# Performance work log

Hardware: AMD Instinct MI355X
Metric: run time of the kernel (lower is better)

Reference implementation:

```python
import jax, jax.numpy as jnp
import numpy as np

N_NODES = 50000
N_EDGES = 500000
D_MODEL = 128
EDGE_DIM = 16
LN_EPS = 1e-5


def setup_inputs() -> dict:
    key = jax.random.key(0)
    ks = jax.random.split(key, 12)
    s = 0.05
    return {
        "x_src": jax.random.normal(ks[0], (N_NODES, D_MODEL), jnp.float32),
        "x_dst": jax.random.normal(ks[1], (N_NODES, D_MODEL), jnp.float32),
        "edge_src": jax.random.randint(ks[2], (N_EDGES,), 0, N_NODES, jnp.int32),
        "edge_dst": jax.random.randint(ks[3], (N_EDGES,), 0, N_NODES, jnp.int32),
        "edge_attr": jax.random.normal(ks[4], (N_EDGES, EDGE_DIM), jnp.float32),
        "W_src": jax.random.normal(ks[5], (D_MODEL, D_MODEL), jnp.float32) * s,
        "W_dst": jax.random.normal(ks[6], (D_MODEL, D_MODEL), jnp.float32) * s,
        "b_dst": jnp.zeros((D_MODEL,), jnp.float32),
        "gate_w1": jax.random.normal(ks[7], (D_MODEL, EDGE_DIM), jnp.float32) * s,
        "gate_b1": jnp.zeros((D_MODEL,), jnp.float32),
        "gate_w2": jax.random.normal(ks[8], (1, D_MODEL), jnp.float32) * s,
        "gate_b2": jnp.zeros((1,), jnp.float32),
        "ln_gamma": jnp.ones((D_MODEL,), jnp.float32),
        "ln_beta": jnp.zeros((D_MODEL,), jnp.float32),
    }


def _layernorm(x, gamma, beta):
    mu = jnp.mean(x, axis=-1, keepdims=True)
    var = jnp.mean(jnp.square(x - mu), axis=-1, keepdims=True)
    return (x - mu) * jax.lax.rsqrt(var + LN_EPS) * gamma + beta


def reference(x_src, x_dst, edge_src, edge_dst, edge_attr,
              W_src, W_dst, b_dst, gate_w1, gate_b1, gate_w2, gate_b2,
              ln_gamma, ln_beta):
    n_dst = x_dst.shape[0]
    # gather + linear message: [E, d]
    msg = jnp.einsum('ed,fd->ef', x_src[edge_src], W_src)
    # edge-gate MLP (norm=False, eval mode -> no dropout): Linear -> gelu -> Linear -> sigmoid
    g = jax.nn.gelu(edge_attr @ gate_w1.T + gate_b1, approximate=False)
    gate = jax.nn.sigmoid(g @ gate_w2.T + gate_b2)  # [E, 1]
    msg = msg * gate
    # scatter-add aggregation and degree normalization
    agg = jax.ops.segment_sum(msg, edge_dst, num_segments=n_dst)
    deg = jax.ops.segment_sum(jnp.ones((edge_dst.shape[0],), msg.dtype), edge_dst,
                              num_segments=n_dst)
    agg = agg / jnp.maximum(deg, 1.0)[:, None]
    out = _layernorm(agg + x_dst @ W_dst.T + b_dst, ln_gamma, ln_beta)
    return jax.nn.gelu(out, approximate=False)
```

## Files before the change

### kernel.cpp

```cpp
#include <hip/hip_runtime.h>

#define D_MODEL 128
#define EDGE_DIM 16

typedef __attribute__((ext_vector_type(8))) short bf16x8;
typedef __attribute__((ext_vector_type(4))) float f32x4;

__device__ __forceinline__ float sigmoid_fast(float a) {
    return 1.0f / (1.0f + __expf(-a));
}
__device__ __forceinline__ float gelu_tanh(float x) {
    float x2  = x * x;
    float arg = x * fmaf(0.07135481627f, x2, 1.59576912161f);
    return x * sigmoid_fast(arg);
}

__device__ __forceinline__ float gelu_poly(float x) {
    float s = fminf(x * x, 2.89f);
    float r = fmaf(-9.4447e-6f, s, 1.154347e-4f);
    r = fmaf(r, s, -1.1873282e-3f);
    r = fmaf(r, s, 9.9735570e-3f);
    r = fmaf(r, s, -6.64903801e-2f);
    r = fmaf(r, s, 3.989422804e-1f);
    return fmaf(s, r, 0.5f * x);
}

__device__ __forceinline__ unsigned short f2bf(float x) {
    unsigned u = __float_as_uint(x);
    u += 0x7FFFu + ((u >> 16) & 1u);
    return (unsigned short)(u >> 16);
}

__global__ __launch_bounds__(256) void wt_kernel(
    const float* __restrict__ Wsrc, const float* __restrict__ Wdst,
    unsigned short* __restrict__ wTfrag)
{
    int i = blockIdx.x * 256 + threadIdx.x;
    if (i >= 8 * 8 * 64) return;
    int kc = i >> 9;
    int ft = (i >> 6) & 7;
    int l  = i & 63;
    int f  = ft * 16 + (l & 15);
    int d0 = kc * 32 + (l >> 4) * 8;
    const float* src = (d0 < D_MODEL) ? (Wsrc + (size_t)f * D_MODEL + d0)
                                      : (Wdst + (size_t)f * D_MODEL + (d0 - D_MODEL));
    unsigned short* dst = wTfrag + (size_t)i * 8;
#pragma unroll
    for (int v = 0; v < 8; v++) dst[v] = f2bf(src[v]);
}

__global__ __launch_bounds__(256) void hist_kernel(
    const int* __restrict__ edst, int* __restrict__ degi, int E)
{
    int e = blockIdx.x * 256 + threadIdx.x;
    if (e < E) atomicAdd(&degi[edst[e]], 1);
}

__global__ __launch_bounds__(256) void scan1_kernel(
    const int* __restrict__ degi, int* __restrict__ starts,
    int* __restrict__ partials, int N)
{
    __shared__ int sm[256];
    int t = threadIdx.x;
    int idx = blockIdx.x * 256 + t;
    int val = (idx < N) ? degi[idx] : 0;
    sm[t] = val;
    __syncthreads();
#pragma unroll
    for (int off = 1; off < 256; off <<= 1) {
        int x = (t >= off) ? sm[t - off] : 0;
        __syncthreads();
        sm[t] += x;
        __syncthreads();
    }
    if (idx < N) starts[idx] = sm[t] - val;
    if (t == 255) partials[blockIdx.x] = sm[255];
}

__global__ __launch_bounds__(256) void scan2_kernel(
    int* __restrict__ partials, int nblocks)
{
    __shared__ int sm[256];
    int t = threadIdx.x;
    int val = (t < nblocks) ? partials[t] : 0;
    sm[t] = val;
    __syncthreads();
#pragma unroll
    for (int off = 1; off < 256; off <<= 1) {
        int x = (t >= off) ? sm[t - off] : 0;
        __syncthreads();
        sm[t] += x;
        __syncthreads();
    }
    if (t < nblocks) partials[t] = sm[t] - val;
}

__global__ __launch_bounds__(256) void scan3_kernel(
    int* __restrict__ starts, int* __restrict__ cursor,
    const int* __restrict__ partials, int N)
{
    int idx = blockIdx.x * 256 + threadIdx.x;
    if (idx < N) {
        int s = starts[idx] + partials[idx >> 8];
        starts[idx] = s;
        cursor[idx] = s;
    }
}

__global__ __launch_bounds__(256) void gate_kernel(
    const float* __restrict__ eattr,
    const float* __restrict__ gw1, const float* __restrict__ gb1,
    const float* __restrict__ gw2, const float* __restrict__ gb2,
    float* __restrict__ gate_out, int E)
{
    int lane = threadIdx.x & 63;
    int wid  = threadIdx.x >> 6;
    int col  = lane & 15;
    int half = lane >> 4;

    bf16x8 bfrag[8];
    float  w2v[8], b1v[8];
#pragma unroll
    for (int jt = 0; jt < 8; jt++) {
        int j = jt * 16 + col;
        w2v[jt] = gw2[j];
        b1v[jt] = gb1[j];
        bf16x8 bf = {0, 0, 0, 0, 0, 0, 0, 0};
        if (half < 2) {
            const float4* wp = (const float4*)(gw1 + j * EDGE_DIM + half * 8);
            float4 u0 = wp[0], u1 = wp[1];
            bf[0] = (short)f2bf(u0.x); bf[1] = (short)f2bf(u0.y);
            bf[2] = (short)f2bf(u0.z); bf[3] = (short)f2bf(u0.w);
            bf[4] = (short)f2bf(u1.x); bf[5] = (short)f2bf(u1.y);
            bf[6] = (short)f2bf(u1.z); bf[7] = (short)f2bf(u1.w);
        }
        bfrag[jt] = bf;
    }
    float b2v = gb2[0];

    int ebase = blockIdx.x * 256 + wid * 64;
    float q[4] = {0.f, 0.f, 0.f, 0.f};

#pragma unroll
    for (int g = 0; g < 4; g++) {
        int e0 = ebase + g * 16;
        if (e0 < E) {
            int e = e0 + col;
            bf16x8 afrag = {0, 0, 0, 0, 0, 0, 0, 0};
            if (half < 2 && e < E) {
                const float4* ap = (const float4*)(eattr + (size_t)e * EDGE_DIM + half * 8);
                float4 a0 = ap[0], a1 = ap[1];
                afrag[0] = (short)f2bf(a0.x); afrag[1] = (short)f2bf(a0.y);
                afrag[2] = (short)f2bf(a0.z); afrag[3] = (short)f2bf(a0.w);
                afrag[4] = (short)f2bf(a1.x); afrag[5] = (short)f2bf(a1.y);
                afrag[6] = (short)f2bf(a1.z); afrag[7] = (short)f2bf(a1.w);
            }

            float p0 = 0.f, p1 = 0.f, p2 = 0.f, p3 = 0.f;
#pragma unroll
            for (int jt = 0; jt < 8; jt++) {
                f32x4 c = {0.f, 0.f, 0.f, 0.f};
                c = __builtin_amdgcn_mfma_f32_16x16x32_bf16(afrag, bfrag[jt], c, 0, 0, 0);
                p0 = fmaf(gelu_poly(c[0] + b1v[jt]), w2v[jt], p0);
                p1 = fmaf(gelu_poly(c[1] + b1v[jt]), w2v[jt], p1);
                p2 = fmaf(gelu_poly(c[2] + b1v[jt]), w2v[jt], p2);
                p3 = fmaf(gelu_poly(c[3] + b1v[jt]), w2v[jt], p3);
            }
#pragma unroll
            for (int m = 8; m >= 1; m >>= 1) {
                p0 += __shfl_xor(p0, m, 64);
                p1 += __shfl_xor(p1, m, 64);
                p2 += __shfl_xor(p2, m, 64);
                p3 += __shfl_xor(p3, m, 64);
            }
            int r3 = lane & 3;
            q[g] = (r3 == 0) ? p0 : (r3 == 1) ? p1 : (r3 == 2) ? p2 : p3;
        }
    }

    int src = ((lane & 15) >> 2) * 16 + (lane & 3);
    float t0 = __shfl(q[0], src, 64);
    float t1 = __shfl(q[1], src, 64);
    float t2 = __shfl(q[2], src, 64);
    float t3 = __shfl(q[3], src, 64);
    int gsel = lane >> 4;
    float logit = (gsel == 0) ? t0 : (gsel == 1) ? t1 : (gsel == 2) ? t2 : t3;
    int e = ebase + lane;
    if (e < E) gate_out[e] = sigmoid_fast(logit + b2v);
}

__global__ __launch_bounds__(256) void scatter_kernel(
    const float* __restrict__ gate_out,
    const int* __restrict__ esrc, const int* __restrict__ edst,
    int* __restrict__ cursor,
    int* __restrict__ sorted_src, float* __restrict__ sorted_gate, int E)
{
    int e = blockIdx.x * 256 + threadIdx.x;
    if (e >= E) return;
    float g = gate_out[e];
    int  dv = edst[e];
    int  sv = esrc[e];
    int pos = atomicAdd(&cursor[dv], 1);
    sorted_src[pos]  = sv;
    sorted_gate[pos] = g;
}

__global__ __launch_bounds__(256) void agg_kernel(
    const float* __restrict__ x_src,
    const int* __restrict__ sorted_src, const float* __restrict__ sorted_gate,
    const int* __restrict__ starts, const int* __restrict__ degi,
    float* __restrict__ h, int N)
{
    int gid  = blockIdx.x * 256 + threadIdx.x;
    int wave = gid >> 6;
    int lane = gid & 63;
    int half = lane >> 5;
    int li   = lane & 31;
    int n    = wave * 2 + half;
    if (n >= N) return;

    int begin = starts[n];
    int cnt   = degi[n];

    float4 accv = make_float4(0.f, 0.f, 0.f, 0.f);
    int i = 0;
    for (; i + 2 <= cnt; i += 2) {
        int   sA = sorted_src[begin + i];
        int   sB = sorted_src[begin + i + 1];
        float gA = sorted_gate[begin + i];
        float gB = sorted_gate[begin + i + 1];
        float4 vA = ((const float4*)(x_src + (size_t)sA * D_MODEL))[li];
        float4 vB = ((const float4*)(x_src + (size_t)sB * D_MODEL))[li];
        accv.x += gA * vA.x + gB * vB.x;
        accv.y += gA * vA.y + gB * vB.y;
        accv.z += gA * vA.z + gB * vB.z;
        accv.w += gA * vA.w + gB * vB.w;
    }
    if (i < cnt) {
        int   s = sorted_src[begin + i];
        float g = sorted_gate[begin + i];
        float4 v = ((const float4*)(x_src + (size_t)s * D_MODEL))[li];
        accv.x += g * v.x;
        accv.y += g * v.y;
        accv.z += g * v.z;
        accv.w += g * v.w;
    }
    float r = 1.0f / (float)max(cnt, 1);
    accv.x *= r; accv.y *= r; accv.z *= r; accv.w *= r;
    *(float4*)(h + (size_t)n * D_MODEL + li * 4) = accv;
}

#define NT 64

__global__ __launch_bounds__(256) void node_kernel(
    const float* __restrict__ h,
    const float* __restrict__ x_dst, const unsigned short* __restrict__ wTfrag,
    const float* __restrict__ bdst, const float* __restrict__ gamma_,
    const float* __restrict__ beta_, float* __restrict__ out, int N)
{
    int lane = threadIdx.x & 63;
    int wid  = threadIdx.x >> 6;
    int col  = lane & 15;
    int half = lane >> 4;
    int base = blockIdx.x * NT + wid * 16;
    if (base >= N) return;

    int arow = base + col;
    bool aok = arow < N;
    const float* hrow = h     + (size_t)arow * D_MODEL + half * 8;
    const float* xrow = x_dst + (size_t)arow * D_MODEL + half * 8;

    f32x4 acc[8];
#pragma unroll
    for (int ft = 0; ft < 8; ft++) acc[ft] = (f32x4){0.f, 0.f, 0.f, 0.f};

    const bf16x8* bbase = ((const bf16x8*)wTfrag) + lane;

#pragma unroll
    for (int kc = 0; kc < 8; kc++) {
        bf16x8 afrag = {0, 0, 0, 0, 0, 0, 0, 0};
        if (aok) {
            const float* ap = (kc < 4) ? (hrow + kc * 32) : (xrow + (kc - 4) * 32);
            float4 a0 = ((const float4*)ap)[0];
            float4 a1 = ((const float4*)ap)[1];
            afrag[0] = (short)f2bf(a0.x); afrag[1] = (short)f2bf(a0.y);
            afrag[2] = (short)f2bf(a0.z); afrag[3] = (short)f2bf(a0.w);
            afrag[4] = (short)f2bf(a1.x); afrag[5] = (short)f2bf(a1.y);
            afrag[6] = (short)f2bf(a1.z); afrag[7] = (short)f2bf(a1.w);
        }
        const bf16x8* bk = bbase + (size_t)kc * 512;
#pragma unroll
        for (int ft = 0; ft < 8; ft++) {
            bf16x8 bfrag = bk[ft * 64];
            acc[ft] = __builtin_amdgcn_mfma_f32_16x16x32_bf16(afrag, bfrag, acc[ft], 0, 0, 0);
        }
    }

    float bv[8], gv[8], ev[8];
#pragma unroll
    for (int ft = 0; ft < 8; ft++) {
        int f = ft * 16 + col;
        bv[ft] = bdst[f];
        gv[ft] = gamma_[f];
        ev[ft] = beta_[f];
    }

#pragma unroll
    for (int r = 0; r < 4; r++) {
        int nr = base + half * 4 + r;
        float yv[8];
        float s1 = 0.f, s2 = 0.f;
#pragma unroll
        for (int ft = 0; ft < 8; ft++) {
            float x = acc[ft][r] + bv[ft];
            yv[ft] = x;
            s1 += x;
            s2 += x * x;
        }
#pragma unroll
        for (int m = 8; m >= 1; m >>= 1) {
            s1 += __shfl_xor(s1, m, 64);
            s2 += __shfl_xor(s2, m, 64);
        }
        float mu   = s1 * (1.0f / 128.0f);
        float var  = s2 * (1.0f / 128.0f) - mu * mu;
        float rstd = rsqrtf(var + 1e-5f);
        if (nr < N) {
            float* op = out + (size_t)nr * D_MODEL + col;
#pragma unroll
            for (int ft = 0; ft < 8; ft++)
                op[ft * 16] = gelu_tanh((yv[ft] - mu) * rstd * gv[ft] + ev[ft]);
        }
    }
}

extern "C" void kernel_launch(void* const* d_in, const int* in_sizes, int n_in,
                              void* d_out, int out_size, void* d_ws, size_t ws_size,
                              hipStream_t stream) {
    const float* x_src  = (const float*)d_in[0];
    const float* x_dst  = (const float*)d_in[1];
    const int*   esrc   = (const int*)d_in[2];
    const int*   edst   = (const int*)d_in[3];
    const float* eattr  = (const float*)d_in[4];
    const float* Wsrc   = (const float*)d_in[5];
    const float* Wdst   = (const float*)d_in[6];
    const float* bdst   = (const float*)d_in[7];
    const float* gw1    = (const float*)d_in[8];
    const float* gb1    = (const float*)d_in[9];
    const float* gw2    = (const float*)d_in[10];
    const float* gb2    = (const float*)d_in[11];
    const float* gamma_ = (const float*)d_in[12];
    const float* beta_  = (const float*)d_in[13];
    float* out = (float*)d_out;

    int E = in_sizes[2];
    int N = in_sizes[1] / D_MODEL;

    char* ws = (char*)d_ws;
    size_t off = 0;
    auto alloc = [&](size_t bytes) {
        size_t cur = off;
        off = (off + bytes + 255) & ~(size_t)255;
        return (void*)(ws + cur);
    };
    unsigned short* wTfrag = (unsigned short*)alloc((size_t)8 * 8 * 64 * 8 * 2);
    int*   degi        = (int*)  alloc((size_t)N * 4);
    int*   starts      = (int*)  alloc((size_t)N * 4);
    int*   cursor      = (int*)  alloc((size_t)N * 4);
    int*   partials    = (int*)  alloc(256 * 4);
    int*   sorted_src  = (int*)  alloc((size_t)E * 4);
    float* sorted_gate = (float*)alloc((size_t)E * 4);
    float* gate_out    = (float*)alloc((size_t)E * 4);
    float* h           = (float*)alloc((size_t)N * D_MODEL * 4);

    int nblocksN = (N + 255) / 256;
    int nblocksE = (E + 255) / 256;

    hipMemsetAsync(degi, 0, (size_t)N * 4, stream);

    wt_kernel<<<16, 256, 0, stream>>>(Wsrc, Wdst, wTfrag);
    gate_kernel<<<nblocksE, 256, 0, stream>>>(
        eattr, gw1, gb1, gw2, gb2, gate_out, E);
    hist_kernel<<<nblocksE, 256, 0, stream>>>(edst, degi, E);
    scan1_kernel<<<nblocksN, 256, 0, stream>>>(degi, starts, partials, N);
    scan2_kernel<<<1, 256, 0, stream>>>(partials, nblocksN);
    scan3_kernel<<<nblocksN, 256, 0, stream>>>(starts, cursor, partials, N);
    scatter_kernel<<<nblocksE, 256, 0, stream>>>(
        gate_out, esrc, edst, cursor, sorted_src, sorted_gate, E);
    agg_kernel<<<((size_t)N * 32 + 255) / 256, 256, 0, stream>>>(
        x_src, sorted_src, sorted_gate, starts, degi, h, N);
    node_kernel<<<(N + NT - 1) / NT, 256, 0, stream>>>(
        h, x_dst, wTfrag, bdst, gamma_, beta_, out, N);
}
```

Before: 271.9 us.

## Gather bf16 copy of x_src in aggregation and store h as bf16

Adds a cast kernel that converts x_src to bf16 once per call, so the edge-gather in agg_kernel reads half the bytes per neighbor row. The aggregation loop is unrolled to four edges, and the aggregated h is written as bf16 so node_kernel loads it directly as MFMA fragments without converting. In exchange there is an extra full pass over x_src (read fp32, write bf16), and the gathered inputs lose precision before accumulation rather than only at the matmul.

```diff
diff --git a/kernel.cpp b/kernel.cpp
--- a/kernel.cpp
+++ b/kernel.cpp
@@ -29,6 +29,24 @@
     unsigned u = __float_as_uint(x);
     u += 0x7FFFu + ((u >> 16) & 1u);
     return (unsigned short)(u >> 16);
+}
+__device__ __forceinline__ float bf2f(unsigned short v) {
+    return __uint_as_float((unsigned)v << 16);
+}
+
+__global__ __launch_bounds__(256) void cast_kernel(
+    const float* __restrict__ x, unsigned short* __restrict__ xb, int total8)
+{
+    int i = blockIdx.x * 256 + threadIdx.x;
+    if (i >= total8) return;
+    const float4* p = (const float4*)(x + (size_t)i * 8);
+    float4 u0 = p[0], u1 = p[1];
+    ushort4 o0, o1;
+    o0.x = f2bf(u0.x); o0.y = f2bf(u0.y); o0.z = f2bf(u0.z); o0.w = f2bf(u0.w);
+    o1.x = f2bf(u1.x); o1.y = f2bf(u1.y); o1.z = f2bf(u1.z); o1.w = f2bf(u1.w);
+    ushort4* q = (ushort4*)(xb + (size_t)i * 8);
+    q[0] = o0;
+    q[1] = o1;
 }
 
 __global__ __launch_bounds__(256) void wt_kernel(
@@ -206,10 +224,10 @@
 }
 
 __global__ __launch_bounds__(256) void agg_kernel(
-    const float* __restrict__ x_src,
+    const unsigned short* __restrict__ xsb,
     const int* __restrict__ sorted_src, const float* __restrict__ sorted_gate,
     const int* __restrict__ starts, const int* __restrict__ degi,
-    float* __restrict__ h, int N)
+    unsigned short* __restrict__ hb, int N)
 {
     int gid  = blockIdx.x * 256 + threadIdx.x;
     int wave = gid >> 6;
@@ -222,38 +240,48 @@
     int begin = starts[n];
     int cnt   = degi[n];
 
-    float4 accv = make_float4(0.f, 0.f, 0.f, 0.f);
+    float a0 = 0.f, a1 = 0.f, a2 = 0.f, a3 = 0.f;
     int i = 0;
-    for (; i + 2 <= cnt; i += 2) {
+    for (; i + 4 <= cnt; i += 4) {
         int   sA = sorted_src[begin + i];
         int   sB = sorted_src[begin + i + 1];
+        int   sC = sorted_src[begin + i + 2];
+        int   sD = sorted_src[begin + i + 3];
         float gA = sorted_gate[begin + i];
         float gB = sorted_gate[begin + i + 1];
-        float4 vA = ((const float4*)(x_src + (size_t)sA * D_MODEL))[li];
-        float4 vB = ((const float4*)(x_src + (size_t)sB * D_MODEL))[li];
-        accv.x += gA * vA.x + gB * vB.x;
-        accv.y += gA * vA.y + gB * vB.y;
-        accv.z += gA * vA.z + gB * vB.z;
-        accv.w += gA * vA.w + gB * vB.w;
-    }
-    if (i < cnt) {
+        float gC = sorted_gate[begin + i + 2];
+        float gD = sorted_gate[begin + i + 3];
+        ushort4 vA = ((const ushort4*)(xsb + (size_t)sA * D_MODEL))[li];
+        ushort4 vB = ((const ushort4*)(xsb + (size_t)sB * D_MODEL))[li];
+        ushort4 vC = ((const ushort4*)(xsb + (size_t)sC * D_MODEL))[li];
+        ushort4 vD = ((const ushort4*)(xsb + (size_t)sD * D_MODEL))[li];
+        a0 += gA * bf2f(vA.x) + gB * bf2f(vB.x) + gC * bf2f(vC.x) + gD * bf2f(vD.x);
+        a1 += gA * bf2f(vA.y) + gB * bf2f(vB.y) + gC * bf2f(vC.y) + gD * bf2f(vD.y);
+        a2 += gA * bf2f(vA.z) + gB * bf2f(vB.z) + gC * bf2f(vC.z) + gD * bf2f(vD.z);
+        a3 += gA * bf2f(vA.w) + gB * bf2f(vB.w) + gC * bf2f(vC.w) + gD * bf2f(vD.w);
+    }
+    for (; i < cnt; i++) {
         int   s = sorted_src[begin + i];
         float g = sorted_gate[begin + i];
-        float4 v = ((const float4*)(x_src + (size_t)s * D_MODEL))[li];
-        accv.x += g * v.x;
-        accv.y += g * v.y;
-        accv.z += g * v.z;
-        accv.w += g * v.w;
+        ushort4 v = ((const ushort4*)(xsb + (size_t)s * D_MODEL))[li];
+        a0 += g * bf2f(v.x);
+        a1 += g * bf2f(v.y);
+        a2 += g * bf2f(v.z);
+        a3 += g * bf2f(v.w);
     }
     float r = 1.0f / (float)max(cnt, 1);
-    accv.x *= r; accv.y *= r; accv.z *= r; accv.w *= r;
-    *(float4*)(h + (size_t)n * D_MODEL + li * 4) = accv;
+    ushort4 o;
+    o.x = f2bf(a0 * r);
+    o.y = f2bf(a1 * r);
+    o.z = f2bf(a2 * r);
+    o.w = f2bf(a3 * r);
+    ((ushort4*)(hb + (size_t)n * D_MODEL))[li] = o;
 }
 
 #define NT 64
 
 __global__ __launch_bounds__(256) void node_kernel(
-    const float* __restrict__ h,
+    const unsigned short* __restrict__ hb,
     const float* __restrict__ x_dst, const unsigned short* __restrict__ wTfrag,
     const float* __restrict__ bdst, const float* __restrict__ gamma_,
     const float* __restrict__ beta_, float* __restrict__ out, int N)
@@ -267,8 +295,8 @@
 
     int arow = base + col;
     bool aok = arow < N;
-    const float* hrow = h     + (size_t)arow * D_MODEL + half * 8;
-    const float* xrow = x_dst + (size_t)arow * D_MODEL + half * 8;
+    const unsigned short* hrow = hb + (size_t)arow * D_MODEL + half * 8;
+    const float*          xrow = x_dst + (size_t)arow * D_MODEL + half * 8;
 
     f32x4 acc[8];
 #pragma unroll
@@ -280,13 +308,17 @@
     for (int kc = 0; kc < 8; kc++) {
         bf16x8 afrag = {0, 0, 0, 0, 0, 0, 0, 0};
         if (aok) {
-            const float* ap = (kc < 4) ? (hrow + kc * 32) : (xrow + (kc - 4) * 32);
-            float4 a0 = ((const float4*)ap)[0];
-            float4 a1 = ((const float4*)ap)[1];
-            afrag[0] = (short)f2bf(a0.x); afrag[1] = (short)f2bf(a0.y);
-            afrag[2] = (short)f2bf(a0.z); afrag[3] = (short)f2bf(a0.w);
-            afrag[4] = (short)f2bf(a1.x); afrag[5] = (short)f2bf(a1.y);
-            afrag[6] = (short)f2bf(a1.z); afrag[7] = (short)f2bf(a1.w);
+            if (kc < 4) {
+                afrag = *(const bf16x8*)(hrow + kc * 32);
+            } else {
+                const float* ap = xrow + (kc - 4) * 32;
+                float4 a0 = ((const float4*)ap)[0];
+                float4 a1 = ((const float4*)ap)[1];
+                afrag[0] = (short)f2bf(a0.x); afrag[1] = (short)f2bf(a0.y);
+                afrag[2] = (short)f2bf(a0.z); afrag[3] = (short)f2bf(a0.w);
+                afrag[4] = (short)f2bf(a1.x); afrag[5] = (short)f2bf(a1.y);
+                afrag[6] = (short)f2bf(a1.z); afrag[7] = (short)f2bf(a1.w);
+            }
         }
         const bf16x8* bk = bbase + (size_t)kc * 512;
 #pragma unroll
@@ -371,14 +403,18 @@
     int*   sorted_src  = (int*)  alloc((size_t)E * 4);
     float* sorted_gate = (float*)alloc((size_t)E * 4);
     float* gate_out    = (float*)alloc((size_t)E * 4);
-    float* h           = (float*)alloc((size_t)N * D_MODEL * 4);
+    unsigned short* xsb = (unsigned short*)alloc((size_t)N * D_MODEL * 2);
+    unsigned short* hb  = (unsigned short*)alloc((size_t)N * D_MODEL * 2);
 
     int nblocksN = (N + 255) / 256;
     int nblocksE = (E + 255) / 256;
+    int total8   = N * (D_MODEL / 8);
+    int nblocksC = (total8 + 255) / 256;
 
     hipMemsetAsync(degi, 0, (size_t)N * 4, stream);
 
     wt_kernel<<<16, 256, 0, stream>>>(Wsrc, Wdst, wTfrag);
+    cast_kernel<<<nblocksC, 256, 0, stream>>>(x_src, xsb, total8);
     gate_kernel<<<nblocksE, 256, 0, stream>>>(
         eattr, gw1, gb1, gw2, gb2, gate_out, E);
     hist_kernel<<<nblocksE, 256, 0, stream>>>(edst, degi, E);
@@ -388,7 +424,7 @@
     scatter_kernel<<<nblocksE, 256, 0, stream>>>(
         gate_out, esrc, edst, cursor, sorted_src, sorted_gate, E);
     agg_kernel<<<((size_t)N * 32 + 255) / 256, 256, 0, stream>>>(
-        x_src, sorted_src, sorted_gate, starts, degi, h, N);
+        xsb, sorted_src, sorted_gate, starts, degi, hb, N);
     node_kernel<<<(N + NT - 1) / NT, 256, 0, stream>>>(
-        h, x_dst, wTfrag, bdst, gamma_, beta_, out, N);
-}
+        hb, x_dst, wTfrag, bdst, gamma_, beta_, out, N);
+}
```

After: 275.4 us. About the same (+1.3%).
